# Performance work log

Hardware: AMD Instinct MI355X
Metric: run time of the kernel (lower is better)

## Reference

```python
import jax, jax.numpy as jnp
import numpy as np

B, T, N = 4, 512, 16
D, H = 256, 8
CTS, CN, CE = 6, 4, 3
TSE, AUXE = 192, 64  # TSE + AUXE == D
DK = D // H


def pe_table(L, d):
    # sinusoidal positional encoding (annotated-transformer style)
    pos = jnp.arange(L, dtype=jnp.float32)[:, None]
    div = jnp.exp(jnp.arange(0, d, 2, dtype=jnp.float32) * (-jnp.log(jnp.float32(10000.0)) / d))
    pe = jnp.zeros((L, d), dtype=jnp.float32)
    pe = pe.at[:, 0::2].set(jnp.sin(pos * div)).at[:, 1::2].set(jnp.cos(pos * div))
    return pe


def setup_inputs() -> dict:
    key = jax.random.key(0)
    ks = jax.random.split(key, 32)
    s = 0.02
    inp = {
        'x': jax.random.normal(ks[0], (B, T, D), jnp.float32),
        'masked_data': jax.random.normal(ks[1], (B, N, CTS, T), jnp.float32),
        'node_aux': jax.random.normal(ks[2], (B, N, CN, T), jnp.float32),
        'edge_aux': jax.random.normal(ks[3], (B, N, CE, T), jnp.float32),
        'attention_mask': jax.random.randint(ks[4], (B, T, N * T), 0, 2, jnp.int32),
        # ts branch
        'W_ts1': jax.random.normal(ks[5], (CTS, TSE)) * s, 'b_ts1': jnp.zeros((TSE,)),
        'W_ts2': jax.random.normal(ks[6], (TSE, TSE)) * s, 'b_ts2': jnp.zeros((TSE,)),
        # node aux branch
        'W_a1': jax.random.normal(ks[7], (CN, AUXE)) * s, 'b_a1': jnp.zeros((AUXE,)),
        'W_a2': jax.random.normal(ks[8], (AUXE, AUXE)) * s, 'b_a2': jnp.zeros((AUXE,)),
        # edge branch
        'W_e1': jax.random.normal(ks[9], (CE, D)) * s, 'b_e1': jnp.zeros((D,)),
        'W_e2': jax.random.normal(ks[10], (D, D)) * s, 'b_e2': jnp.zeros((D,)),
        # multi-head cross-attention
        'Wq': jax.random.normal(ks[11], (D, D)) * s, 'bq': jnp.zeros((D,)),
        'Wk': jax.random.normal(ks[12], (D, D)) * s, 'bk': jnp.zeros((D,)),
        'Wv': jax.random.normal(ks[13], (D, D)) * s, 'bv': jnp.zeros((D,)),
        'Wo': jax.random.normal(ks[14], (D, D)) * s, 'bo': jnp.zeros((D,)),
        # sublayer layernorm
        'ln_g': jnp.ones((D,)), 'ln_b': jnp.zeros((D,)),
    }
    return inp


def reference(x, masked_data, node_aux, edge_aux, attention_mask,
              W_ts1, b_ts1, W_ts2, b_ts2, W_a1, b_a1, W_a2, b_a2,
              W_e1, b_e1, W_e2, b_e2, Wq, bq, Wk, bk, Wv, bv, Wo, bo,
              ln_g, ln_b):
    pe = pe_table(T, D)  # [T, D]
    xq = x + pe[None]  # pe applied to query sequence (dropout=identity in eval)

    # per-neighbor ts MLP: transpose [B,N,C,T] -> [B,N,T,C], two Linears with ReLU between
    ts = jax.nn.relu(jnp.einsum('bnct,ce->bnte', masked_data, W_ts1) + b_ts1)
    ts = ts @ W_ts2 + b_ts2  # [B,N,T,TSE]
    aux = jax.nn.relu(jnp.einsum('bnct,ce->bnte', node_aux, W_a1) + b_a1)
    aux = aux @ W_a2 + b_a2  # [B,N,T,AUXE]
    nbr = jnp.concatenate([ts, aux], axis=-1)  # [B,N,T,D]

    edge = jax.nn.relu(jnp.einsum('bnct,cd->bntd', edge_aux, W_e1) + b_e1)
    edge = edge @ W_e2 + b_e2  # [B,N,T,D]

    # PE applied per neighbor (positions restart each neighbor), then concat over kv seq
    keys = (nbr * edge + pe[None, None]).reshape(B, N * T, D)
    vals = (nbr + pe[None, None]).reshape(B, N * T, D)

    # SublayerConnection: xq + attn(LayerNorm(xq), keys, vals, mask)
    mu = xq.mean(-1, keepdims=True)
    var = ((xq - mu) ** 2).mean(-1, keepdims=True)
    xn = (xq - mu) / jnp.sqrt(var + 1e-6) * ln_g + ln_b

    q = (xn @ Wq + bq).reshape(B, T, H, DK).transpose(0, 2, 1, 3)        # [B,H,T,DK]
    k = (keys @ Wk + bk).reshape(B, N * T, H, DK).transpose(0, 2, 1, 3)  # [B,H,NT,DK]
    v = (vals @ Wv + bv).reshape(B, N * T, H, DK).transpose(0, 2, 1, 3)

    scores = jnp.einsum('bhqd,bhkd->bhqk', q, k) / jnp.sqrt(jnp.float32(DK))
    scores = jnp.where(attention_mask[:, None, :, :] == 0, jnp.float32(-1e9), scores)
    attn = jax.nn.softmax(scores, axis=-1)
    ctx = jnp.einsum('bhqk,bhkd->bhqd', attn, v).transpose(0, 2, 1, 3).reshape(B, T, D)
    out = ctx @ Wo + bo
    return xq + out
```

## Files before the change

### kernel.cpp

```cpp
#include <hip/hip_runtime.h>
#include <hip/hip_bf16.h>

#define B_ 4
#define T_ 512
#define N_ 16
#define D_ 256
#define H_ 8
#define DK_ 32
#define NT_ (N_ * T_)
#define CTS_ 6
#define CN_ 4
#define CE_ 3
#define TSE_ 192
#define AUXE_ 64
#define SPLIT_ 8
#define KWORDS_ (NT_ / 64)

#define QSCALE_ 0.2550689747f

#define HTS_S 204
#define HAUX_S 76
#define HED_S 268
#define SK_S 268

typedef unsigned long long ull;
typedef unsigned int uint;
typedef __bf16 bf16x8 __attribute__((ext_vector_type(8)));
typedef float f32x4 __attribute__((ext_vector_type(4)));
typedef float f32x16 __attribute__((ext_vector_type(16)));

__global__ __launch_bounds__(256) void pe_kernel(float* pe) {
    int t = blockIdx.x;
    int d = threadIdx.x;
    int j = d >> 1;
    float div = expf((float)(2 * j) * (-9.210340371976184f / 256.0f));
    float a = (float)t * div;
    pe[t * D_ + d] = (d & 1) ? cosf(a) : sinf(a);
}

__global__ __launch_bounds__(256) void maskbits_kernel(const int* __restrict__ mask,
                                                       ull* __restrict__ bitsT) {
    int row = blockIdx.x;
    int b = row >> 9, t = row & (T_ - 1);
    const int* mrow = mask + (size_t)row * NT_;
    int lane = threadIdx.x & 63, wave = threadIdx.x >> 6;
    for (int it = 0; it < NT_ / 256; ++it) {
        int k = it * 256 + wave * 64 + lane;
        ull bal = __ballot(mrow[k] != 0);
        if (lane == 0) bitsT[((size_t)b * KWORDS_ + (k >> 6)) * T_ + t] = bal;
    }
}

__global__ __launch_bounds__(256) void wprep_kernel(
    const float* __restrict__ W_ts1, const float* __restrict__ W_a1,
    const float* __restrict__ W_e1, const float* __restrict__ W_ts2,
    const float* __restrict__ W_a2, const float* __restrict__ W_e2,
    const float* __restrict__ Wk, const float* __restrict__ Wv,
    const float* __restrict__ Wq, const float* __restrict__ Wo,
    __bf16* __restrict__ ts1P, __bf16* __restrict__ a1P, __bf16* __restrict__ e1P,
    __bf16* __restrict__ ts2T, __bf16* __restrict__ a2T, __bf16* __restrict__ e2T,
    __bf16* __restrict__ WkT, __bf16* __restrict__ WvT,
    __bf16* __restrict__ WqT, __bf16* __restrict__ WoT) {
    int i = blockIdx.x * 256 + threadIdx.x;
    if (i < 6144) { int col = i >> 5, k = i & 31;
        ts1P[i] = (__bf16)(k < 6 ? W_ts1[k * TSE_ + col] : 0.f); return; }
    i -= 6144;
    if (i < 2048) { int col = i >> 5, k = i & 31;
        a1P[i] = (__bf16)((k >= 6 && k < 10) ? W_a1[(k - 6) * AUXE_ + col] : 0.f); return; }
    i -= 2048;
    if (i < 8192) { int col = i >> 5, k = i & 31;
        e1P[i] = (__bf16)((k >= 10 && k < 13) ? W_e1[(k - 10) * D_ + col] : 0.f); return; }
    i -= 8192;
    if (i < 36864) {
        int tile = i >> 9, lr = (i >> 5) & 15, kk = i & 31;
        int ct = tile / 6, ks = tile % 6;
        ts2T[i] = (__bf16)W_ts2[(ks * 32 + kk) * TSE_ + ct * 16 + lr]; return; }
    i -= 36864;
    if (i < 4096) {
        int tile = i >> 9, lr = (i >> 5) & 15, kk = i & 31;
        int ct = tile / 2, ks = tile % 2;
        a2T[i] = (__bf16)W_a2[(ks * 32 + kk) * AUXE_ + ct * 16 + lr]; return; }
    i -= 4096;
    if (i < 65536) {
        int tile = i >> 9, lr = (i >> 5) & 15, kk = i & 31;
        int ct = tile >> 3, ks = tile & 7;
        e2T[i] = (__bf16)W_e2[(ks * 32 + kk) * D_ + ct * 16 + lr]; return; }
    i -= 65536;
    if (i < 65536) {
        int tile = i >> 9, lr = (i >> 5) & 15, kk = i & 31;
        int ct = tile >> 3, ks = tile & 7;
        WkT[i] = (__bf16)Wk[(ks * 32 + kk) * D_ + ct * 16 + lr]; return; }
    i -= 65536;
    if (i < 65536) {
        int tile = i >> 9, lr = (i >> 5) & 15, kk = i & 31;
        int ct = tile >> 3, ks = tile & 7;
        WvT[i] = (__bf16)Wv[(ks * 32 + kk) * D_ + ct * 16 + lr]; return; }
    i -= 65536;
    if (i < 65536) {
        int tile = i >> 9, lr = (i >> 5) & 15, kk = i & 31;
        int ct = tile >> 3, ks = tile & 7;
        WqT[i] = (__bf16)(Wq[(ks * 32 + kk) * D_ + ct * 16 + lr] * QSCALE_); return; }
    i -= 65536;
    {
        int tile = i >> 9, lr = (i >> 5) & 15, kk = i & 31;
        int ct = tile >> 3, ks = tile & 7;
        WoT[i] = (__bf16)Wo[(ks * 32 + kk) * D_ + ct * 16 + lr]; }
}

__global__ __launch_bounds__(256, 4) void kv_mfma_kernel(
    const float* __restrict__ md, const float* __restrict__ na, const float* __restrict__ ea,
    const __bf16* __restrict__ ts1P, const __bf16* __restrict__ a1P,
    const __bf16* __restrict__ e1P,
    const float* __restrict__ b_ts1, const float* __restrict__ b_a1,
    const float* __restrict__ b_e1,
    const __bf16* __restrict__ ts2T, const __bf16* __restrict__ a2T,
    const __bf16* __restrict__ e2T,
    const float* __restrict__ b_ts2, const float* __restrict__ b_a2,
    const float* __restrict__ b_e2,
    const __bf16* __restrict__ WkT, const float* __restrict__ bk,
    const __bf16* __restrict__ WvT, const float* __restrict__ bv,
    const float* __restrict__ pe, __bf16* __restrict__ Kb, __bf16* __restrict__ Vf) {
    int blk = blockIdx.x;
    int t0 = (blk & 15) * 32;
    int n = (blk >> 4) & 15;
    int b = blk >> 8;
    int tid = threadIdx.x, lane = tid & 63;
    int wq = tid >> 6;
    int lr = lane & 15, lg = lane >> 4;

    __shared__ __bf16 sA[32 * 40];
    __shared__ __bf16 sU[17536];
    __bf16* hts = sU;
    __bf16* haux = sU + 6528;
    __bf16* hedge = sU + 8960;
    __bf16* skey = sU;
    __bf16* sval = sU + 8576;

    for (int i = tid; i < 32 * 40; i += 256) sA[i] = (__bf16)0.f;
    __syncthreads();
    {
        int t = tid & 31, c0 = tid >> 5;
        size_t bn = (size_t)b * N_ + n;
        for (int c = c0; c < 13; c += 8) {
            float v;
            if (c < 6) v = md[(bn * CTS_ + c) * T_ + t0 + t];
            else if (c < 10) v = na[(bn * CN_ + (c - 6)) * T_ + t0 + t];
            else v = ea[(bn * CE_ + (c - 10)) * T_ + t0 + t];
            sA[t * 40 + c] = (__bf16)v;
        }
    }
    __syncthreads();

    int foff = lr * 32 + lg * 8;
    f32x4 z4 = {0.f, 0.f, 0.f, 0.f};
    bf16x8 a1f0 = *(const bf16x8*)(sA + lr * 40 + lg * 8);
    bf16x8 a1f1 = *(const bf16x8*)(sA + (16 + lr) * 40 + lg * 8);
    int crow0 = lg * 4;

    {
        bool isTs = (wq < 3);
#pragma unroll
        for (int i = 0; i < 4; ++i) {
            int ctn = wq * 4 + i;
            const __bf16* src = isTs ? (ts1P + ctn * 512) : (a1P + (ctn - 12) * 512);
            bf16x8 bf = *(const bf16x8*)(src + foff);
            f32x4 c0 = __builtin_amdgcn_mfma_f32_16x16x32_bf16(a1f0, bf, z4, 0, 0, 0);
            f32x4 c1 = __builtin_amdgcn_mfma_f32_16x16x32_bf16(a1f1, bf, z4, 0, 0, 0);
            if (isTs) {
                int gcol = ctn * 16 + lr;
                float bias = b_ts1[gcol];
#pragma unroll
                for (int r = 0; r < 4; ++r) {
                    hts[(crow0 + r) * HTS_S + gcol] = (__bf16)fmaxf(c0[r] + bias, 0.f);
                    hts[(16 + crow0 + r) * HTS_S + gcol] = (__bf16)fmaxf(c1[r] + bias, 0.f);
                }
            } else {
                int acol = (ctn - 12) * 16 + lr;
                float bias = b_a1[acol];
#pragma unroll
                for (int r = 0; r < 4; ++r) {
                    haux[(crow0 + r) * HAUX_S + acol] = (__bf16)fmaxf(c0[r] + bias, 0.f);
                    haux[(16 + crow0 + r) * HAUX_S + acol] = (__bf16)fmaxf(c1[r] + bias, 0.f);
                }
            }
        }
#pragma unroll
        for (int i = 0; i < 4; ++i) {
            int cte = wq * 4 + i;
            bf16x8 bf = *(const bf16x8*)(e1P + cte * 512 + foff);
            f32x4 c0 = __builtin_amdgcn_mfma_f32_16x16x32_bf16(a1f0, bf, z4, 0, 0, 0);
            f32x4 c1 = __builtin_amdgcn_mfma_f32_16x16x32_bf16(a1f1, bf, z4, 0, 0, 0);
            int gcol = cte * 16 + lr;
            float bias = b_e1[gcol];
#pragma unroll
            for (int r = 0; r < 4; ++r) {
                hedge[(crow0 + r) * HED_S + gcol] = (__bf16)fmaxf(c0[r] + bias, 0.f);
                hedge[(16 + crow0 + r) * HED_S + gcol] = (__bf16)fmaxf(c1[r] + bias, 0.f);
            }
        }
    }
    __syncthreads();

    f32x4 eacc[2][4];
#pragma unroll
    for (int i = 0; i < 4; ++i) { eacc[0][i] = z4; eacc[1][i] = z4; }
    {
        const __bf16* ebase = e2T + (size_t)(wq * 4) * 8 * 512 + foff;
        bf16x8 bcur[4];
#pragma unroll
        for (int i = 0; i < 4; ++i) bcur[i] = *(const bf16x8*)(ebase + i * 4096);
#pragma unroll 1
        for (int ks = 0; ks < 8; ++ks) {
            bf16x8 bnext[4];
            if (ks < 7) {
#pragma unroll
                for (int i = 0; i < 4; ++i)
                    bnext[i] = *(const bf16x8*)(ebase + i * 4096 + (ks + 1) * 512);
            }
            __builtin_amdgcn_sched_barrier(0);
            bf16x8 af0 = *(const bf16x8*)(hedge + lr * HED_S + ks * 32 + lg * 8);
            bf16x8 af1 = *(const bf16x8*)(hedge + (16 + lr) * HED_S + ks * 32 + lg * 8);
#pragma unroll
            for (int i = 0; i < 4; ++i) {
                eacc[0][i] = __builtin_amdgcn_mfma_f32_16x16x32_bf16(af0, bcur[i], eacc[0][i], 0, 0, 0);
                eacc[1][i] = __builtin_amdgcn_mfma_f32_16x16x32_bf16(af1, bcur[i], eacc[1][i], 0, 0, 0);
            }
            if (ks < 7) {
#pragma unroll
                for (int i = 0; i < 4; ++i) bcur[i] = bnext[i];
            }
        }
    }

    f32x4 nacc[2][4];
#pragma unroll
    for (int i = 0; i < 4; ++i) { nacc[0][i] = z4; nacc[1][i] = z4; }
    if (wq < 3) {
        const __bf16* nbase = ts2T + (size_t)(wq * 4) * 6 * 512 + foff;
        bf16x8 bcur[4];
#pragma unroll
        for (int i = 0; i < 4; ++i) bcur[i] = *(const bf16x8*)(nbase + i * 3072);
#pragma unroll 1
        for (int ks = 0; ks < 6; ++ks) {
            bf16x8 bnext[4];
            if (ks < 5) {
#pragma unroll
                for (int i = 0; i < 4; ++i)
                    bnext[i] = *(const bf16x8*)(nbase + i * 3072 + (ks + 1) * 512);
            }
            __builtin_amdgcn_sched_barrier(0);
            bf16x8 af0 = *(const bf16x8*)(hts + lr * HTS_S + ks * 32 + lg * 8);
            bf16x8 af1 = *(const bf16x8*)(hts + (16 + lr) * HTS_S + ks * 32 + lg * 8);
#pragma unroll
            for (int i = 0; i < 4; ++i) {
                nacc[0][i] = __builtin_amdgcn_mfma_f32_16x16x32_bf16(af0, bcur[i], nacc[0][i], 0, 0, 0);
                nacc[1][i] = __builtin_amdgcn_mfma_f32_16x16x32_bf16(af1, bcur[i], nacc[1][i], 0, 0, 0);
            }
            if (ks < 5) {
#pragma unroll
                for (int i = 0; i < 4; ++i) bcur[i] = bnext[i];
            }
        }
    } else {
#pragma unroll
        for (int ks = 0; ks < 2; ++ks) {
            bf16x8 af0 = *(const bf16x8*)(haux + lr * HAUX_S + ks * 32 + lg * 8);
            bf16x8 af1 = *(const bf16x8*)(haux + (16 + lr) * HAUX_S + ks * 32 + lg * 8);
#pragma unroll
            for (int i = 0; i < 4; ++i) {
                bf16x8 bf = *(const bf16x8*)(a2T + (i * 2 + ks) * 512 + foff);
                nacc[0][i] = __builtin_amdgcn_mfma_f32_16x16x32_bf16(af0, bf, nacc[0][i], 0, 0, 0);
                nacc[1][i] = __builtin_amdgcn_mfma_f32_16x16x32_bf16(af1, bf, nacc[1][i], 0, 0, 0);
            }
        }
    }
    __syncthreads();

#pragma unroll
    for (int i = 0; i < 4; ++i) {
        int gcol = wq * 64 + i * 16 + lr;
        float nb_bias = (wq < 3) ? b_ts2[gcol] : b_a2[gcol - 192];
        float ed_bias = b_e2[gcol];
#pragma unroll
        for (int rf = 0; rf < 2; ++rf)
#pragma unroll
            for (int r = 0; r < 4; ++r) {
                int row = rf * 16 + crow0 + r;
                float p = pe[(t0 + row) * D_ + gcol];
                float nb = nacc[rf][i][r] + nb_bias;
                float ed = eacc[rf][i][r] + ed_bias;
                skey[row * SK_S + gcol] = (__bf16)(nb * ed + p);
                sval[row * SK_S + gcol] = (__bf16)(nb + p);
            }
    }
    __syncthreads();

    size_t key0 = (size_t)n * T_ + t0;

    {
        const __bf16* kbse = WkT + (size_t)(wq * 4) * 8 * 512 + foff;
        f32x4 ka[2][4];
#pragma unroll
        for (int i = 0; i < 4; ++i) { ka[0][i] = z4; ka[1][i] = z4; }
        bf16x8 bcur[4];
#pragma unroll
        for (int i = 0; i < 4; ++i) bcur[i] = *(const bf16x8*)(kbse + i * 4096);
#pragma unroll 1
        for (int ks = 0; ks < 8; ++ks) {
            bf16x8 bnext[4];
            if (ks < 7) {
#pragma unroll
                for (int i = 0; i < 4; ++i)
                    bnext[i] = *(const bf16x8*)(kbse + i * 4096 + (ks + 1) * 512);
            }
            __builtin_amdgcn_sched_barrier(0);
            bf16x8 af0 = *(const bf16x8*)(skey + lr * SK_S + ks * 32 + lg * 8);
            bf16x8 af1 = *(const bf16x8*)(skey + (16 + lr) * SK_S + ks * 32 + lg * 8);
#pragma unroll
            for (int i = 0; i < 4; ++i) {
                ka[0][i] = __builtin_amdgcn_mfma_f32_16x16x32_bf16(af0, bcur[i], ka[0][i], 0, 0, 0);
                ka[1][i] = __builtin_amdgcn_mfma_f32_16x16x32_bf16(af1, bcur[i], ka[1][i], 0, 0, 0);
            }
            if (ks < 7) {
#pragma unroll
                for (int i = 0; i < 4; ++i) bcur[i] = bnext[i];
            }
        }
#pragma unroll
        for (int i = 0; i < 4; ++i) {
            int gcol = wq * 64 + i * 16 + lr;
            float kbias = bk[gcol];
            int h = gcol >> 5, dd = gcol & 31;
            size_t bh = (size_t)b * H_ + h;
#pragma unroll
            for (int rf = 0; rf < 2; ++rf) {
                int crow = rf * 16 + crow0;
#pragma unroll
                for (int r = 0; r < 4; ++r)
                    Kb[(bh * NT_ + key0 + crow + r) * DK_ + dd] = (__bf16)(ka[rf][i][r] + kbias);
            }
        }
    }

    {
        const __bf16* vbse = WvT + (size_t)(wq * 4) * 8 * 512 + foff;
        f32x4 va[2][4];
#pragma unroll
        for (int i = 0; i < 4; ++i) { va[0][i] = z4; va[1][i] = z4; }
        bf16x8 bcur[4];
#pragma unroll
        for (int i = 0; i < 4; ++i) bcur[i] = *(const bf16x8*)(vbse + i * 4096);
#pragma unroll 1
        for (int ks = 0; ks < 8; ++ks) {
            bf16x8 bnext[4];
            if (ks < 7) {
#pragma unroll
                for (int i = 0; i < 4; ++i)
                    bnext[i] = *(const bf16x8*)(vbse + i * 4096 + (ks + 1) * 512);
            }
            __builtin_amdgcn_sched_barrier(0);
            bf16x8 af0 = *(const bf16x8*)(sval + lr * SK_S + ks * 32 + lg * 8);
            bf16x8 af1 = *(const bf16x8*)(sval + (16 + lr) * SK_S + ks * 32 + lg * 8);
#pragma unroll
            for (int i = 0; i < 4; ++i) {
                va[0][i] = __builtin_amdgcn_mfma_f32_16x16x32_bf16(af0, bcur[i], va[0][i], 0, 0, 0);
                va[1][i] = __builtin_amdgcn_mfma_f32_16x16x32_bf16(af1, bcur[i], va[1][i], 0, 0, 0);
            }
            if (ks < 7) {
#pragma unroll
                for (int i = 0; i < 4; ++i) bcur[i] = bnext[i];
            }
        }
#pragma unroll
        for (int i = 0; i < 4; ++i) {
            int gcol = wq * 64 + i * 16 + lr;
            float vbias = bv[gcol];
            int h = gcol >> 5, dd = gcol & 31;
            size_t bh = (size_t)b * H_ + h;
#pragma unroll
            for (int rf = 0; rf < 2; ++rf) {
                int crow = rf * 16 + crow0;
                __bf16 tmp[4];
#pragma unroll
                for (int r = 0; r < 4; ++r) tmp[r] = (__bf16)(va[rf][i][r] + vbias);
                size_t kg = key0 + crow;
                int within = (int)(kg & 63);
                int vks = within >> 4, vl5 = (within >> 3) & 1, j0 = within & 7;
                size_t tile = kg >> 6;
                size_t vaddr = ((bh * (NT_ / 64) + tile) * 4 + vks) * 512 +
                               (size_t)(vl5 * 32 + dd) * 8 + j0;
                *(ushort4*)(Vf + vaddr) = *(ushort4*)tmp;
            }
        }
    }
}

__global__ __launch_bounds__(256) void q_mfma_kernel(
    const float* __restrict__ x, const float* __restrict__ pe,
    const __bf16* __restrict__ WqT, const float* __restrict__ bq,
    const float* __restrict__ ln_g, const float* __restrict__ ln_b,
    __bf16* __restrict__ Qb) {
    int blk = blockIdx.x;
    int t0 = (blk & 15) * 32;
    int b = blk >> 4;
    int tid = threadIdx.x, lane = tid & 63;
    int wq = tid >> 6, lr = lane & 15, lg = lane >> 4;

    __shared__ __bf16 s_xn[32 * SK_S];

    {
        int row = tid >> 3, sub = tid & 7;
        size_t roff = ((size_t)b * T_ + t0 + row) * D_;
        const float* pr = pe + (t0 + row) * D_;
        f32x4 vv[8];
        float s1 = 0.f, s2 = 0.f;
#pragma unroll
        for (int q4 = 0; q4 < 8; ++q4) {
            int c = q4 * 32 + sub * 4;
            f32x4 xv = *(const f32x4*)(x + roff + c);
            f32x4 pv = *(const f32x4*)(pr + c);
            f32x4 t4;
#pragma unroll
            for (int j = 0; j < 4; ++j) {
                t4[j] = xv[j] + pv[j];
                s1 += t4[j];
                s2 += t4[j] * t4[j];
            }
            vv[q4] = t4;
        }
#pragma unroll
        for (int o = 1; o <= 4; o <<= 1) {
            s1 += __shfl_xor(s1, o, 64);
            s2 += __shfl_xor(s2, o, 64);
        }
        float mu = s1 * (1.f / D_);
        float var = s2 * (1.f / D_) - mu * mu;
        float rs = rsqrtf(var + 1e-6f);
#pragma unroll
        for (int q4 = 0; q4 < 8; ++q4) {
            int c = q4 * 32 + sub * 4;
            f32x4 g4 = *(const f32x4*)(ln_g + c);
            f32x4 b4 = *(const f32x4*)(ln_b + c);
#pragma unroll
            for (int j = 0; j < 4; ++j)
                s_xn[row * SK_S + c + j] = (__bf16)((vv[q4][j] - mu) * rs * g4[j] + b4[j]);
        }
    }
    __syncthreads();

    int foff = lr * 32 + lg * 8;
    int crow0 = lg * 4;
    f32x4 z4 = {0.f, 0.f, 0.f, 0.f};
    f32x4 qa[2][4];
#pragma unroll
    for (int i = 0; i < 4; ++i) { qa[0][i] = z4; qa[1][i] = z4; }
    const __bf16* qbse = WqT + (size_t)(wq * 4) * 8 * 512 + foff;
#pragma unroll
    for (int ks = 0; ks < 8; ++ks) {
        bf16x8 af0 = *(const bf16x8*)(s_xn + lr * SK_S + ks * 32 + lg * 8);
        bf16x8 af1 = *(const bf16x8*)(s_xn + (16 + lr) * SK_S + ks * 32 + lg * 8);
#pragma unroll
        for (int i = 0; i < 4; ++i) {
            bf16x8 b8 = *(const bf16x8*)(qbse + i * 4096 + ks * 512);
            qa[0][i] = __builtin_amdgcn_mfma_f32_16x16x32_bf16(af0, b8, qa[0][i], 0, 0, 0);
            qa[1][i] = __builtin_amdgcn_mfma_f32_16x16x32_bf16(af1, b8, qa[1][i], 0, 0, 0);
        }
    }
#pragma unroll
    for (int i = 0; i < 4; ++i) {
        int gcol = wq * 64 + i * 16 + lr;
        float bias = bq[gcol] * QSCALE_;
#pragma unroll
        for (int rf = 0; rf < 2; ++rf)
#pragma unroll
            for (int r = 0; r < 4; ++r)
                Qb[((size_t)b * T_ + t0 + rf * 16 + crow0 + r) * D_ + gcol] =
                    (__bf16)(qa[rf][i][r] + bias);
    }
}

__global__ __launch_bounds__(256, 4) void attn_mfma_kernel(
    const __bf16* __restrict__ Qb, const __bf16* __restrict__ Kb,
    const __bf16* __restrict__ Vf, const ull* __restrict__ bitsT,
    float* __restrict__ Opart, float* __restrict__ Lpart) {
    int blk = blockIdx.x;
    int kh = blk & (SPLIT_ - 1);
    int qt = (blk >> 3) & 3;
    int h = (blk >> 5) & 7;
    int b = blk >> 8;
    int tid = threadIdx.x, lane = tid & 63, w = tid >> 6;
    int lq = lane & 31, l5 = lane >> 5;

    const size_t bh = (size_t)b * H_ + h;
    const int TILES = KWORDS_ / SPLIT_;

    int qglob = qt * 128 + w * 32 + lq;
    const __bf16* qbase = Qb + ((size_t)b * T_ + qglob) * D_ + h * DK_ + l5 * 8;
    bf16x8 qf0 = *(const bf16x8*)(qbase);
    bf16x8 qf1 = *(const bf16x8*)(qbase + 16);

    const __bf16* kp = Kb + bh * NT_ * DK_ + (size_t)(kh * TILES) * 64 * DK_;
    const __bf16* vp = Vf + (bh * (NT_ / 64) + (size_t)(kh * TILES)) * 2048;
    const ull* mp = bitsT + (size_t)b * KWORDS_ * T_ + (size_t)(kh * TILES) * T_ + qglob;

    int k00 = lq * DK_ + l5 * 8;
    int k01 = k00 + 16;
    int k10 = (32 + lq) * DK_ + l5 * 8;
    int k11 = k10 + 16;
    int shamt = 4 * l5;

    f32x16 acc, acc_l, zv;
#pragma unroll
    for (int i = 0; i < 16; ++i) { acc[i] = 0.f; acc_l[i] = 0.f; zv[i] = 0.f; }
    union { uint u[4]; bf16x8 v; } onesf;
    onesf.u[0] = 0x3F803F80u; onesf.u[1] = 0x3F803F80u;
    onesf.u[2] = 0x3F803F80u; onesf.u[3] = 0x3F803F80u;

    bf16x8 kc0 = *(const bf16x8*)(kp + k00);
    bf16x8 kc1 = *(const bf16x8*)(kp + k01);
    bf16x8 kc2 = *(const bf16x8*)(kp + k10);
    bf16x8 kc3 = *(const bf16x8*)(kp + k11);
    ull mw = *mp;

#pragma unroll 1
    for (int kt = 0; kt < TILES; ++kt) {
        bf16x8 vc0 = *(const bf16x8*)(vp + 0 * 512 + lane * 8);
        bf16x8 vc1 = *(const bf16x8*)(vp + 1 * 512 + lane * 8);
        bf16x8 vc2 = *(const bf16x8*)(vp + 2 * 512 + lane * 8);
        bf16x8 vc3 = *(const bf16x8*)(vp + 3 * 512 + lane * 8);
        bf16x8 kn0, kn1, kn2, kn3;
        ull mn = 0;
        if (kt + 1 < TILES) {
            kn0 = *(const bf16x8*)(kp + 2048 + k00);
            kn1 = *(const bf16x8*)(kp + 2048 + k01);
            kn2 = *(const bf16x8*)(kp + 2048 + k10);
            kn3 = *(const bf16x8*)(kp + 2048 + k11);
            mn = mp[T_];
        }
        __builtin_amdgcn_sched_barrier(0);

        ull sh = mw >> shamt;

#pragma unroll
        for (int s = 0; s < 2; ++s) {
            f32x16 sc = __builtin_amdgcn_mfma_f32_32x32x16_bf16(
                s ? kc2 : kc0, qf0, zv, 0, 0, 0);
            sc = __builtin_amdgcn_mfma_f32_32x32x16_bf16(
                s ? kc3 : kc1, qf1, sc, 0, 0, 0);

            uint ms = (uint)(sh >> (32 * s));
            float p[16];
#pragma unroll
            for (int r = 0; r < 16; ++r) {
                int pos = (r & 3) + 8 * (r >> 2);
                float e = __builtin_amdgcn_exp2f(sc[r]);
                int mb = __builtin_amdgcn_sbfe((int)ms, (uint)pos, 1u);
                p[r] = __uint_as_float(__float_as_uint(e) & (uint)mb);
            }

#pragma unroll
            for (int h2 = 0; h2 < 2; ++h2) {
                uint w0, w1, w2, w3;
                asm("v_cvt_pk_bf16_f32 %0, %1, %2" : "=v"(w0) : "v"(p[8 * h2 + 0]), "v"(p[8 * h2 + 1]));
                asm("v_cvt_pk_bf16_f32 %0, %1, %2" : "=v"(w1) : "v"(p[8 * h2 + 2]), "v"(p[8 * h2 + 3]));
                asm("v_cvt_pk_bf16_f32 %0, %1, %2" : "=v"(w2) : "v"(p[8 * h2 + 4]), "v"(p[8 * h2 + 5]));
                asm("v_cvt_pk_bf16_f32 %0, %1, %2" : "=v"(w3) : "v"(p[8 * h2 + 6]), "v"(p[8 * h2 + 7]));
                asm volatile("v_permlane32_swap_b32 %0, %1" : "+v"(w0), "+v"(w2));
                asm volatile("v_permlane32_swap_b32 %0, %1" : "+v"(w1), "+v"(w3));
                union { uint u[4]; bf16x8 v; } pa;
                pa.u[0] = w0; pa.u[1] = w1; pa.u[2] = w2; pa.u[3] = w3;
                bf16x8 vfr = (s == 0) ? (h2 == 0 ? vc0 : vc1) : (h2 == 0 ? vc2 : vc3);
                acc = __builtin_amdgcn_mfma_f32_32x32x16_bf16(pa.v, vfr, acc, 0, 0, 0);
                acc_l = __builtin_amdgcn_mfma_f32_32x32x16_bf16(pa.v, onesf.v, acc_l, 0, 0, 0);
            }
        }

        kp += 2048;
        vp += 2048;
        mp += T_;
        if (kt + 1 < TILES) {
            kc0 = kn0; kc1 = kn1; kc2 = kn2; kc3 = kn3;
            mw = mn;
        }
    }

    size_t obase = (((size_t)kh * B_ + b) * H_ + h) * T_ + qt * 128 + w * 32;
#pragma unroll
    for (int r = 0; r < 16; ++r) {
        int q = (r & 3) + 8 * (r >> 2) + 4 * l5;
        Opart[(obase + q) * DK_ + lq] = acc[r];
    }
    if (lq == 0) {
#pragma unroll
        for (int r = 0; r < 16; ++r) {
            int q = (r & 3) + 8 * (r >> 2) + 4 * l5;
            Lpart[obase + q] = acc_l[r];
        }
    }
}

__global__ __launch_bounds__(256) void out_mfma_kernel(
    const float* __restrict__ Opart, const float* __restrict__ Lpart,
    const float* __restrict__ x, const float* __restrict__ pe,
    const __bf16* __restrict__ WoT, const float* __restrict__ bo,
    float* __restrict__ out) {
    int blk = blockIdx.x;
    int t0 = (blk & 15) * 32;
    int b = blk >> 4;
    int tid = threadIdx.x, lane = tid & 63;
    int wq = tid >> 6, lr = lane & 15, lg = lane >> 4;

    __shared__ __bf16 sc_[32 * SK_S];
    __shared__ float sLinv[32 * 8];
    size_t ps = (size_t)B_ * H_ * T_;

    {
        int row = tid >> 3, hh = tid & 7;
        size_t base = ((size_t)b * H_ + hh) * T_ + t0 + row;
        float L = 0.f;
#pragma unroll
        for (int s = 0; s < SPLIT_; ++s) L += Lpart[s * ps + base];
        sLinv[row * 8 + hh] = 1.0f / L;
    }
    __syncthreads();

    for (int idx = tid; idx < 32 * 64; idx += 256) {
        int r = idx >> 6, g = idx & 63;
        int hh = g >> 3, d4 = (g & 7) * 4;
        size_t base = (((size_t)b * H_ + hh) * T_ + t0 + r) * DK_ + d4;
        f32x4 o = {0.f, 0.f, 0.f, 0.f};
#pragma unroll
        for (int s = 0; s < SPLIT_; ++s) {
            f32x4 t4 = *(const f32x4*)(Opart + s * ps * DK_ + base);
            o[0] += t4[0]; o[1] += t4[1]; o[2] += t4[2]; o[3] += t4[3];
        }
        float li = sLinv[r * 8 + hh];
        int c = hh * 32 + d4;
#pragma unroll
        for (int j = 0; j < 4; ++j) sc_[r * SK_S + c + j] = (__bf16)(o[j] * li);
    }
    __syncthreads();

    int foff = lr * 32 + lg * 8;
    int crow0 = lg * 4;
    f32x4 z4 = {0.f, 0.f, 0.f, 0.f};
    f32x4 oa[2][4];
#pragma unroll
    for (int i = 0; i < 4; ++i) { oa[0][i] = z4; oa[1][i] = z4; }
    const __bf16* obse = WoT + (size_t)(wq * 4) * 8 * 512 + foff;
#pragma unroll
    for (int ks = 0; ks < 8; ++ks) {
        bf16x8 af0 = *(const bf16x8*)(sc_ + lr * SK_S + ks * 32 + lg * 8);
        bf16x8 af1 = *(const bf16x8*)(sc_ + (16 + lr) * SK_S + ks * 32 + lg * 8);
#pragma unroll
        for (int i = 0; i < 4; ++i) {
            bf16x8 b8 = *(const bf16x8*)(obse + i * 4096 + ks * 512);
            oa[0][i] = __builtin_amdgcn_mfma_f32_16x16x32_bf16(af0, b8, oa[0][i], 0, 0, 0);
            oa[1][i] = __builtin_amdgcn_mfma_f32_16x16x32_bf16(af1, b8, oa[1][i], 0, 0, 0);
        }
    }
#pragma unroll
    for (int i = 0; i < 4; ++i) {
        int gcol = wq * 64 + i * 16 + lr;
        float bias = bo[gcol];
#pragma unroll
        for (int rf = 0; rf < 2; ++rf)
#pragma unroll
            for (int r = 0; r < 4; ++r) {
                int t = t0 + rf * 16 + crow0 + r;
                size_t off = ((size_t)b * T_ + t) * D_ + gcol;
                out[off] = x[off] + pe[t * D_ + gcol] + oa[rf][i][r] + bias;
            }
    }
}

extern "C" void kernel_launch(void* const* d_in, const int* in_sizes, int n_in,
                              void* d_out, int out_size, void* d_ws, size_t ws_size,
                              hipStream_t stream) {
    const float* x = (const float*)d_in[0];
    const float* md = (const float*)d_in[1];
    const float* na = (const float*)d_in[2];
    const float* ea = (const float*)d_in[3];
    const int* mask = (const int*)d_in[4];
    const float* W_ts1 = (const float*)d_in[5];
    const float* b_ts1 = (const float*)d_in[6];
    const float* W_ts2 = (const float*)d_in[7];
    const float* b_ts2 = (const float*)d_in[8];
    const float* W_a1 = (const float*)d_in[9];
    const float* b_a1 = (const float*)d_in[10];
    const float* W_a2 = (const float*)d_in[11];
    const float* b_a2 = (const float*)d_in[12];
    const float* W_e1 = (const float*)d_in[13];
    const float* b_e1 = (const float*)d_in[14];
    const float* W_e2 = (const float*)d_in[15];
    const float* b_e2 = (const float*)d_in[16];
    const float* Wq = (const float*)d_in[17];
    const float* bq = (const float*)d_in[18];
    const float* Wk = (const float*)d_in[19];
    const float* bk = (const float*)d_in[20];
    const float* Wv = (const float*)d_in[21];
    const float* bv = (const float*)d_in[22];
    const float* Wo = (const float*)d_in[23];
    const float* bo = (const float*)d_in[24];
    const float* ln_g = (const float*)d_in[25];
    const float* ln_b = (const float*)d_in[26];
    float* out = (float*)d_out;

    char* ws = (char*)d_ws;
    float* pe = (float*)ws;     ws += (size_t)T_ * D_ * 4;
    ull* bitsT = (ull*)ws;      ws += (size_t)B_ * KWORDS_ * T_ * 8;
    __bf16* Kb = (__bf16*)ws;   ws += (size_t)B_ * H_ * NT_ * DK_ * 2;
    __bf16* Vf = (__bf16*)ws;   ws += (size_t)B_ * H_ * NT_ * DK_ * 2;
    __bf16* Qb = (__bf16*)ws;   ws += (size_t)B_ * T_ * D_ * 2;
    float* Opart = (float*)ws;  ws += (size_t)SPLIT_ * B_ * H_ * T_ * DK_ * 4;
    float* Lpart = (float*)ws;  ws += (size_t)SPLIT_ * B_ * H_ * T_ * 4;
    __bf16* ts1P = (__bf16*)ws; ws += 6144 * 2;
    __bf16* a1P = (__bf16*)ws;  ws += 2048 * 2;
    __bf16* e1P = (__bf16*)ws;  ws += 8192 * 2;
    __bf16* ts2T = (__bf16*)ws; ws += 36864 * 2;
    __bf16* a2T = (__bf16*)ws;  ws += 4096 * 2;
    __bf16* e2T = (__bf16*)ws;  ws += 65536 * 2;
    __bf16* WkT = (__bf16*)ws;  ws += 65536 * 2;
    __bf16* WvT = (__bf16*)ws;  ws += 65536 * 2;
    __bf16* WqT = (__bf16*)ws;  ws += 65536 * 2;
    __bf16* WoT = (__bf16*)ws;  ws += 65536 * 2;

    pe_kernel<<<T_, 256, 0, stream>>>(pe);
    maskbits_kernel<<<B_ * T_, 256, 0, stream>>>(mask, bitsT);
    wprep_kernel<<<1504, 256, 0, stream>>>(W_ts1, W_a1, W_e1, W_ts2, W_a2, W_e2,
                                           Wk, Wv, Wq, Wo,
                                           ts1P, a1P, e1P, ts2T, a2T, e2T,
                                           WkT, WvT, WqT, WoT);
    kv_mfma_kernel<<<B_ * N_ * (T_ / 32), 256, 0, stream>>>(
        md, na, ea, ts1P, a1P, e1P, b_ts1, b_a1, b_e1,
        ts2T, a2T, e2T, b_ts2, b_a2, b_e2, WkT, bk, WvT, bv, pe, Kb, Vf);
    q_mfma_kernel<<<B_ * (T_ / 32), 256, 0, stream>>>(x, pe, WqT, bq, ln_g, ln_b, Qb);
    attn_mfma_kernel<<<B_ * H_ * (T_ / 128) * SPLIT_, 256, 0, stream>>>(
        Qb, Kb, Vf, bitsT, Opart, Lpart);
    out_mfma_kernel<<<B_ * (T_ / 32), 256, 0, stream>>>(Opart, Lpart, x, pe, WoT, bo, out);
}
```

Measured before the change: 124.9 us.

## Halve kv kernel row tile to 16 rows and double occupancy

The KV-projection kernel now processes 16 time steps per block instead of 32, so the grid doubles, LDS use per block halves and per-thread accumulators shrink from 2x4 to 4 fragments. Launch bounds move from 4 to 8 blocks per SM to exploit the lower register and LDS footprint. The software prefetch of B fragments in the edge and ts second-layer loops is removed in favour of direct loads. The cost is that each weight fragment loaded from global memory now feeds only one MFMA instead of two, doubling weight traffic per output row.

```diff
diff --git a/kernel.cpp b/kernel.cpp
--- a/kernel.cpp
+++ b/kernel.cpp
@@ -107,7 +107,7 @@
         WoT[i] = (__bf16)Wo[(ks * 32 + kk) * D_ + ct * 16 + lr]; }
 }
 
-__global__ __launch_bounds__(256, 4) void kv_mfma_kernel(
+__global__ __launch_bounds__(256, 8) void kv_mfma_kernel(
     const float* __restrict__ md, const float* __restrict__ na, const float* __restrict__ ea,
     const __bf16* __restrict__ ts1P, const __bf16* __restrict__ a1P,
     const __bf16* __restrict__ e1P,
@@ -121,40 +121,37 @@
     const __bf16* __restrict__ WvT, const float* __restrict__ bv,
     const float* __restrict__ pe, __bf16* __restrict__ Kb, __bf16* __restrict__ Vf) {
     int blk = blockIdx.x;
-    int t0 = (blk & 15) * 32;
-    int n = (blk >> 4) & 15;
-    int b = blk >> 8;
+    int t0 = (blk & 31) * 16;
+    int n = (blk >> 5) & 15;
+    int b = blk >> 9;
     int tid = threadIdx.x, lane = tid & 63;
     int wq = tid >> 6;
     int lr = lane & 15, lg = lane >> 4;
 
-    __shared__ __bf16 sA[32 * 40];
-    __shared__ __bf16 sU[17536];
+    __shared__ __bf16 sA[16 * 40];
+    __shared__ __bf16 sU[8768];
     __bf16* hts = sU;
-    __bf16* haux = sU + 6528;
-    __bf16* hedge = sU + 8960;
+    __bf16* haux = sU + 3264;
+    __bf16* hedge = sU + 4480;
     __bf16* skey = sU;
-    __bf16* sval = sU + 8576;
-
-    for (int i = tid; i < 32 * 40; i += 256) sA[i] = (__bf16)0.f;
-    __syncthreads();
-    {
-        int t = tid & 31, c0 = tid >> 5;
+    __bf16* sval = sU + 4288;
+
+    for (int i = tid; i < 16 * 40; i += 256) sA[i] = (__bf16)0.f;
+    __syncthreads();
+    if (tid < 208) {
+        int c = tid >> 4, t = tid & 15;
         size_t bn = (size_t)b * N_ + n;
-        for (int c = c0; c < 13; c += 8) {
-            float v;
-            if (c < 6) v = md[(bn * CTS_ + c) * T_ + t0 + t];
-            else if (c < 10) v = na[(bn * CN_ + (c - 6)) * T_ + t0 + t];
-            else v = ea[(bn * CE_ + (c - 10)) * T_ + t0 + t];
-            sA[t * 40 + c] = (__bf16)v;
-        }
+        float v;
+        if (c < 6) v = md[(bn * CTS_ + c) * T_ + t0 + t];
+        else if (c < 10) v = na[(bn * CN_ + (c - 6)) * T_ + t0 + t];
+        else v = ea[(bn * CE_ + (c - 10)) * T_ + t0 + t];
+        sA[t * 40 + c] = (__bf16)v;
     }
     __syncthreads();
 
     int foff = lr * 32 + lg * 8;
     f32x4 z4 = {0.f, 0.f, 0.f, 0.f};
-    bf16x8 a1f0 = *(const bf16x8*)(sA + lr * 40 + lg * 8);
-    bf16x8 a1f1 = *(const bf16x8*)(sA + (16 + lr) * 40 + lg * 8);
+    bf16x8 a1f = *(const bf16x8*)(sA + lr * 40 + lg * 8);
     int crow0 = lg * 4;
 
     {
@@ -164,113 +161,73 @@
             int ctn = wq * 4 + i;
             const __bf16* src = isTs ? (ts1P + ctn * 512) : (a1P + (ctn - 12) * 512);
             bf16x8 bf = *(const bf16x8*)(src + foff);
-            f32x4 c0 = __builtin_amdgcn_mfma_f32_16x16x32_bf16(a1f0, bf, z4, 0, 0, 0);
-            f32x4 c1 = __builtin_amdgcn_mfma_f32_16x16x32_bf16(a1f1, bf, z4, 0, 0, 0);
+            f32x4 c0 = __builtin_amdgcn_mfma_f32_16x16x32_bf16(a1f, bf, z4, 0, 0, 0);
             if (isTs) {
                 int gcol = ctn * 16 + lr;
                 float bias = b_ts1[gcol];
 #pragma unroll
-                for (int r = 0; r < 4; ++r) {
+                for (int r = 0; r < 4; ++r)
                     hts[(crow0 + r) * HTS_S + gcol] = (__bf16)fmaxf(c0[r] + bias, 0.f);
-                    hts[(16 + crow0 + r) * HTS_S + gcol] = (__bf16)fmaxf(c1[r] + bias, 0.f);
-                }
             } else {
                 int acol = (ctn - 12) * 16 + lr;
                 float bias = b_a1[acol];
 #pragma unroll
-                for (int r = 0; r < 4; ++r) {
+                for (int r = 0; r < 4; ++r)
                     haux[(crow0 + r) * HAUX_S + acol] = (__bf16)fmaxf(c0[r] + bias, 0.f);
-                    haux[(16 + crow0 + r) * HAUX_S + acol] = (__bf16)fmaxf(c1[r] + bias, 0.f);
-                }
             }
         }
 #pragma unroll
         for (int i = 0; i < 4; ++i) {
             int cte = wq * 4 + i;
             bf16x8 bf = *(const bf16x8*)(e1P + cte * 512 + foff);
-            f32x4 c0 = __builtin_amdgcn_mfma_f32_16x16x32_bf16(a1f0, bf, z4, 0, 0, 0);
-            f32x4 c1 = __builtin_amdgcn_mfma_f32_16x16x32_bf16(a1f1, bf, z4, 0, 0, 0);
+            f32x4 c0 = __builtin_amdgcn_mfma_f32_16x16x32_bf16(a1f, bf, z4, 0, 0, 0);
             int gcol = cte * 16 + lr;
             float bias = b_e1[gcol];
 #pragma unroll
-            for (int r = 0; r < 4; ++r) {
+            for (int r = 0; r < 4; ++r)
                 hedge[(crow0 + r) * HED_S + gcol] = (__bf16)fmaxf(c0[r] + bias, 0.f);
-                hedge[(16 + crow0 + r) * HED_S + gcol] = (__bf16)fmaxf(c1[r] + bias, 0.f);
-            }
-        }
-    }
-    __syncthreads();
-
-    f32x4 eacc[2][4];
-#pragma unroll
-    for (int i = 0; i < 4; ++i) { eacc[0][i] = z4; eacc[1][i] = z4; }
+        }
+    }
+    __syncthreads();
+
+    f32x4 eacc[4];
+#pragma unroll
+    for (int i = 0; i < 4; ++i) eacc[i] = z4;
     {
         const __bf16* ebase = e2T + (size_t)(wq * 4) * 8 * 512 + foff;
-        bf16x8 bcur[4];
-#pragma unroll
-        for (int i = 0; i < 4; ++i) bcur[i] = *(const bf16x8*)(ebase + i * 4096);
 #pragma unroll 1
         for (int ks = 0; ks < 8; ++ks) {
-            bf16x8 bnext[4];
-            if (ks < 7) {
-#pragma unroll
-                for (int i = 0; i < 4; ++i)
-                    bnext[i] = *(const bf16x8*)(ebase + i * 4096 + (ks + 1) * 512);
-            }
-            __builtin_amdgcn_sched_barrier(0);
-            bf16x8 af0 = *(const bf16x8*)(hedge + lr * HED_S + ks * 32 + lg * 8);
-            bf16x8 af1 = *(const bf16x8*)(hedge + (16 + lr) * HED_S + ks * 32 + lg * 8);
+            bf16x8 af = *(const bf16x8*)(hedge + lr * HED_S + ks * 32 + lg * 8);
 #pragma unroll
             for (int i = 0; i < 4; ++i) {
-                eacc[0][i] = __builtin_amdgcn_mfma_f32_16x16x32_bf16(af0, bcur[i], eacc[0][i], 0, 0, 0);
-                eacc[1][i] = __builtin_amdgcn_mfma_f32_16x16x32_bf16(af1, bcur[i], eacc[1][i], 0, 0, 0);
-            }
-            if (ks < 7) {
-#pragma unroll
-                for (int i = 0; i < 4; ++i) bcur[i] = bnext[i];
-            }
-        }
-    }
-
-    f32x4 nacc[2][4];
-#pragma unroll
-    for (int i = 0; i < 4; ++i) { nacc[0][i] = z4; nacc[1][i] = z4; }
+                bf16x8 bf = *(const bf16x8*)(ebase + i * 4096 + ks * 512);
+                eacc[i] = __builtin_amdgcn_mfma_f32_16x16x32_bf16(af, bf, eacc[i], 0, 0, 0);
+            }
+        }
+    }
+
+    f32x4 nacc[4];
+#pragma unroll
+    for (int i = 0; i < 4; ++i) nacc[i] = z4;
     if (wq < 3) {
         const __bf16* nbase = ts2T + (size_t)(wq * 4) * 6 * 512 + foff;
-        bf16x8 bcur[4];
-#pragma unroll
-        for (int i = 0; i < 4; ++i) bcur[i] = *(const bf16x8*)(nbase + i * 3072);
 #pragma unroll 1
         for (int ks = 0; ks < 6; ++ks) {
-            bf16x8 bnext[4];
-            if (ks < 5) {
-#pragma unroll
-                for (int i = 0; i < 4; ++i)
-                    bnext[i] = *(const bf16x8*)(nbase + i * 3072 + (ks + 1) * 512);
-            }
-            __builtin_amdgcn_sched_barrier(0);
-            bf16x8 af0 = *(const bf16x8*)(hts + lr * HTS_S + ks * 32 + lg * 8);
-            bf16x8 af1 = *(const bf16x8*)(hts + (16 + lr) * HTS_S + ks * 32 + lg * 8);
+            bf16x8 af = *(const bf16x8*)(hts + lr * HTS_S + ks * 32 + lg * 8);
 #pragma unroll
             for (int i = 0; i < 4; ++i) {
-                nacc[0][i] = __builtin_amdgcn_mfma_f32_16x16x32_bf16(af0, bcur[i], nacc[0][i], 0, 0, 0);
-                nacc[1][i] = __builtin_amdgcn_mfma_f32_16x16x32_bf16(af1, bcur[i], nacc[1][i], 0, 0, 0);
-            }
-            if (ks < 5) {
-#pragma unroll
-                for (int i = 0; i < 4; ++i) bcur[i] = bnext[i];
+                bf16x8 bf = *(const bf16x8*)(nbase + i * 3072 + ks * 512);
+                nacc[i] = __builtin_amdgcn_mfma_f32_16x16x32_bf16(af, bf, nacc[i], 0, 0, 0);
             }
         }
     } else {
 #pragma unroll
         for (int ks = 0; ks < 2; ++ks) {
-            bf16x8 af0 = *(const bf16x8*)(haux + lr * HAUX_S + ks * 32 + lg * 8);
-            bf16x8 af1 = *(const bf16x8*)(haux + (16 + lr) * HAUX_S + ks * 32 + lg * 8);
+            bf16x8 af = *(const bf16x8*)(haux + lr * HAUX_S + ks * 32 + lg * 8);
 #pragma unroll
             for (int i = 0; i < 4; ++i) {
                 bf16x8 bf = *(const bf16x8*)(a2T + (i * 2 + ks) * 512 + foff);
-                nacc[0][i] = __builtin_amdgcn_mfma_f32_16x16x32_bf16(af0, bf, nacc[0][i], 0, 0, 0);
-                nacc[1][i] = __builtin_amdgcn_mfma_f32_16x16x32_bf16(af1, bf, nacc[1][i], 0, 0, 0);
+                nacc[i] = __builtin_amdgcn_mfma_f32_16x16x32_bf16(af, bf, nacc[i], 0, 0, 0);
             }
         }
     }
@@ -282,16 +239,14 @@
         float nb_bias = (wq < 3) ? b_ts2[gcol] : b_a2[gcol - 192];
         float ed_bias = b_e2[gcol];
 #pragma unroll
-        for (int rf = 0; rf < 2; ++rf)
-#pragma unroll
-            for (int r = 0; r < 4; ++r) {
-                int row = rf * 16 + crow0 + r;
-                float p = pe[(t0 + row) * D_ + gcol];
-                float nb = nacc[rf][i][r] + nb_bias;
-                float ed = eacc[rf][i][r] + ed_bias;
-                skey[row * SK_S + gcol] = (__bf16)(nb * ed + p);
-                sval[row * SK_S + gcol] = (__bf16)(nb + p);
-            }
+        for (int r = 0; r < 4; ++r) {
+            int row = crow0 + r;
+            float p = pe[(t0 + row) * D_ + gcol];
+            float nb = nacc[i][r] + nb_bias;
+            float ed = eacc[i][r] + ed_bias;
+            skey[row * SK_S + gcol] = (__bf16)(nb * ed + p);
+            sval[row * SK_S + gcol] = (__bf16)(nb + p);
+        }
     }
     __syncthreads();
 
@@ -299,9 +254,9 @@
 
     {
         const __bf16* kbse = WkT + (size_t)(wq * 4) * 8 * 512 + foff;
-        f32x4 ka[2][4];
-#pragma unroll
-        for (int i = 0; i < 4; ++i) { ka[0][i] = z4; ka[1][i] = z4; }
+        f32x4 ka[4];
+#pragma unroll
+        for (int i = 0; i < 4; ++i) ka[i] = z4;
         bf16x8 bcur[4];
 #pragma unroll
         for (int i = 0; i < 4; ++i) bcur[i] = *(const bf16x8*)(kbse + i * 4096);
@@ -314,13 +269,10 @@
                     bnext[i] = *(const bf16x8*)(kbse + i * 4096 + (ks + 1) * 512);
             }
             __builtin_amdgcn_sched_barrier(0);
-            bf16x8 af0 = *(const bf16x8*)(skey + lr * SK_S + ks * 32 + lg * 8);
-            bf16x8 af1 = *(const bf16x8*)(skey + (16 + lr) * SK_S + ks * 32 + lg * 8);
-#pragma unroll
-            for (int i = 0; i < 4; ++i) {
-                ka[0][i] = __builtin_amdgcn_mfma_f32_16x16x32_bf16(af0, bcur[i], ka[0][i], 0, 0, 0);
-                ka[1][i] = __builtin_amdgcn_mfma_f32_16x16x32_bf16(af1, bcur[i], ka[1][i], 0, 0, 0);
-            }
+            bf16x8 af = *(const bf16x8*)(skey + lr * SK_S + ks * 32 + lg * 8);
+#pragma unroll
+            for (int i = 0; i < 4; ++i)
+                ka[i] = __builtin_amdgcn_mfma_f32_16x16x32_bf16(af, bcur[i], ka[i], 0, 0, 0);
             if (ks < 7) {
 #pragma unroll
                 for (int i = 0; i < 4; ++i) bcur[i] = bnext[i];
@@ -333,20 +285,16 @@
             int h = gcol >> 5, dd = gcol & 31;
             size_t bh = (size_t)b * H_ + h;
 #pragma unroll
-            for (int rf = 0; rf < 2; ++rf) {
-                int crow = rf * 16 + crow0;
-#pragma unroll
-                for (int r = 0; r < 4; ++r)
-                    Kb[(bh * NT_ + key0 + crow + r) * DK_ + dd] = (__bf16)(ka[rf][i][r] + kbias);
-            }
+            for (int r = 0; r < 4; ++r)
+                Kb[(bh * NT_ + key0 + crow0 + r) * DK_ + dd] = (__bf16)(ka[i][r] + kbias);
         }
     }
 
     {
         const __bf16* vbse = WvT + (size_t)(wq * 4) * 8 * 512 + foff;
-        f32x4 va[2][4];
-#pragma unroll
-        for (int i = 0; i < 4; ++i) { va[0][i] = z4; va[1][i] = z4; }
+        f32x4 va[4];
+#pragma unroll
+        for (int i = 0; i < 4; ++i) va[i] = z4;
         bf16x8 bcur[4];
 #pragma unroll
         for (int i = 0; i < 4; ++i) bcur[i] = *(const bf16x8*)(vbse + i * 4096);
@@ -359,13 +307,10 @@
                     bnext[i] = *(const bf16x8*)(vbse + i * 4096 + (ks + 1) * 512);
             }
             __builtin_amdgcn_sched_barrier(0);
-            bf16x8 af0 = *(const bf16x8*)(sval + lr * SK_S + ks * 32 + lg * 8);
-            bf16x8 af1 = *(const bf16x8*)(sval + (16 + lr) * SK_S + ks * 32 + lg * 8);
-#pragma unroll
-            for (int i = 0; i < 4; ++i) {
-                va[0][i] = __builtin_amdgcn_mfma_f32_16x16x32_bf16(af0, bcur[i], va[0][i], 0, 0, 0);
-                va[1][i] = __builtin_amdgcn_mfma_f32_16x16x32_bf16(af1, bcur[i], va[1][i], 0, 0, 0);
-            }
+            bf16x8 af = *(const bf16x8*)(sval + lr * SK_S + ks * 32 + lg * 8);
+#pragma unroll
+            for (int i = 0; i < 4; ++i)
+                va[i] = __builtin_amdgcn_mfma_f32_16x16x32_bf16(af, bcur[i], va[i], 0, 0, 0);
             if (ks < 7) {
 #pragma unroll
                 for (int i = 0; i < 4; ++i) bcur[i] = bnext[i];
@@ -377,20 +322,16 @@
             float vbias = bv[gcol];
             int h = gcol >> 5, dd = gcol & 31;
             size_t bh = (size_t)b * H_ + h;
-#pragma unroll
-            for (int rf = 0; rf < 2; ++rf) {
-                int crow = rf * 16 + crow0;
-                __bf16 tmp[4];
-#pragma unroll
-                for (int r = 0; r < 4; ++r) tmp[r] = (__bf16)(va[rf][i][r] + vbias);
-                size_t kg = key0 + crow;
-                int within = (int)(kg & 63);
-                int vks = within >> 4, vl5 = (within >> 3) & 1, j0 = within & 7;
-                size_t tile = kg >> 6;
-                size_t vaddr = ((bh * (NT_ / 64) + tile) * 4 + vks) * 512 +
-                               (size_t)(vl5 * 32 + dd) * 8 + j0;
-                *(ushort4*)(Vf + vaddr) = *(ushort4*)tmp;
-            }
+            __bf16 tmp[4];
+#pragma unroll
+            for (int r = 0; r < 4; ++r) tmp[r] = (__bf16)(va[i][r] + vbias);
+            size_t kg = key0 + crow0;
+            int within = (int)(kg & 63);
+            int vks = within >> 4, vl5 = (within >> 3) & 1, j0 = within & 7;
+            size_t tile = kg >> 6;
+            size_t vaddr = ((bh * (NT_ / 64) + tile) * 4 + vks) * 512 +
+                           (size_t)(vl5 * 32 + dd) * 8 + j0;
+            *(ushort4*)(Vf + vaddr) = *(ushort4*)tmp;
         }
     }
 }
@@ -731,7 +672,7 @@
                                            Wk, Wv, Wq, Wo,
                                            ts1P, a1P, e1P, ts2T, a2T, e2T,
                                            WkT, WvT, WqT, WoT);
-    kv_mfma_kernel<<<B_ * N_ * (T_ / 32), 256, 0, stream>>>(
+    kv_mfma_kernel<<<B_ * N_ * (T_ / 16), 256, 0, stream>>>(
         md, na, ea, ts1P, a1P, e1P, b_ts1, b_a1, b_e1,
         ts2T, a2T, e2T, b_ts2, b_a2, b_e2, WkT, bk, WvT, bv, pe, Kb, Vf);
     q_mfma_kernel<<<B_ * (T_ / 32), 256, 0, stream>>>(x, pe, WqT, bq, ln_g, ln_b, Qb);
```

New measurement: 150.1 us. 1.2x slower.
